# Optimization experiments

Measured on AMD Instinct MI355X. Metric: run time of the kernel, lower is better.

The kernel has to match this reference:

```python
import jax, jax.numpy as jnp
import numpy as np
from jax import lax


def ste_round(x):
    # straight-through round (Brevitas fake-quant)
    return x + lax.stop_gradient(jnp.round(x) - x)


def ste_binary(w):
    # straight-through binarization to {-1, +1}
    b = jnp.where(w >= 0, 1.0, -1.0).astype(w.dtype)
    return w + lax.stop_gradient(b - w)


def quant_identity_2b(x, s):
    # signed 2-bit fake quant: levels {-2,-1,0,1} * s
    return jnp.clip(ste_round(x / s), -2.0, 1.0) * s


def quant_relu_2b(x, s):
    # unsigned 2-bit fake quant after ReLU: levels {0,1,2,3} * s
    return jnp.clip(ste_round(jax.nn.relu(x) / s), 0.0, 3.0) * s


def binary_weight(w, s):
    return ste_binary(w) * s


def conv2d(x, w):
    return lax.conv_general_dilated(x, w, (1, 1), 'VALID',
                                    dimension_numbers=('NCHW', 'OIHW', 'NCHW'))


def maxpool2(x):
    return lax.reduce_window(x, -jnp.inf, lax.max, (1, 1, 2, 2), (1, 1, 2, 2), 'VALID')


def scale_bias(x, scale, bias):
    # BatchNorm2dToQuantScaleBias at inference: per-channel affine
    return x * scale[None, :, None, None] + bias[None, :, None, None]


def setup_inputs() -> dict:
    key = jax.random.key(0)
    ks = jax.random.split(key, 16)
    B = 16384
    d = {
        'x': jax.random.normal(ks[0], (B, 3, 32, 32), jnp.float32),
        'w1': jax.random.normal(ks[1], (6, 3, 5, 5), jnp.float32) * 0.1,
        'b1': jax.random.normal(ks[2], (6,), jnp.float32) * 0.01,
        'w2': jax.random.normal(ks[3], (16, 6, 5, 5), jnp.float32) * 0.1,
        'b2': jax.random.normal(ks[4], (16,), jnp.float32) * 0.01,
        'fw1': jax.random.normal(ks[5], (100, 400), jnp.float32) * 0.05,
        'fb1': jax.random.normal(ks[6], (100,), jnp.float32) * 0.01,
        'fw2': jax.random.normal(ks[7], (50, 100), jnp.float32) * 0.05,
        'fb2': jax.random.normal(ks[8], (50,), jnp.float32) * 0.01,
        'fw3': jax.random.normal(ks[9], (10, 50), jnp.float32) * 0.05,
        'fb3': jax.random.normal(ks[10], (10,), jnp.float32) * 0.01,
        'bn1_scale': jax.random.uniform(ks[11], (6,), jnp.float32, 0.5, 1.5),
        'bn1_bias': jax.random.normal(ks[12], (6,), jnp.float32) * 0.1,
        'bn2_scale': jax.random.uniform(ks[13], (16,), jnp.float32, 0.5, 1.5),
        'bn2_bias': jax.random.normal(ks[14], (16,), jnp.float32) * 0.1,
        's_in': jnp.float32(1.0),
        's_w1': jnp.float32(0.1),
        's_w2': jnp.float32(0.1),
        's_fw1': jnp.float32(0.05),
        's_fw2': jnp.float32(0.05),
        's_fw3': jnp.float32(0.05),
        's_a1': jnp.float32(0.5),
        's_a2': jnp.float32(0.5),
        's_a3': jnp.float32(0.5),
        's_a4': jnp.float32(0.5),
    }
    return d


def reference(x, w1, b1, w2, b2, fw1, fb1, fw2, fb2, fw3, fb3,
              bn1_scale, bn1_bias, bn2_scale, bn2_bias,
              s_in, s_w1, s_w2, s_fw1, s_fw2, s_fw3,
              s_a1, s_a2, s_a3, s_a4):
    # quant_inp (signed 2-bit)
    x = quant_identity_2b(x, s_in)
    # qconv1 (binary weights) -> pool -> BN scale-bias -> 2-bit ReLU
    x = conv2d(x, binary_weight(w1, s_w1)) + b1[None, :, None, None]   # [B,6,28,28]
    x = scale_bias(maxpool2(x), bn1_scale, bn1_bias)                   # [B,6,14,14]
    x = quant_relu_2b(x, s_a1)
    # qconv2 -> BN -> pool -> 2-bit ReLU (pool and BN commute as in code: BN2(pool2(...)))
    x = conv2d(x, binary_weight(w2, s_w2)) + b2[None, :, None, None]   # [B,16,10,10]
    x = scale_bias(maxpool2(x), bn2_scale, bn2_bias)                   # [B,16,5,5]
    x = quant_relu_2b(x, s_a2)
    # flatten -> binary FCs with 2-bit ReLUs
    x = x.reshape(x.shape[0], -1)                                      # [B,400]
    x = quant_relu_2b(x @ binary_weight(fw1, s_fw1).T + fb1, s_a3)     # [B,100]
    x = quant_relu_2b(x @ binary_weight(fw2, s_fw2).T + fb2, s_a4)     # [B,50]
    x = x @ binary_weight(fw3, s_fw3).T + fb3                          # [B,10]
    return x
```

## Files before the change

### kernel.cpp

```cpp
#include <hip/hip_runtime.h>
#include <stdint.h>

typedef uint32_t u32;

#if defined(__has_builtin) && __has_builtin(__builtin_amdgcn_sdot4)
#define SDOT4(a,b,c) __builtin_amdgcn_sdot4((int)(a),(int)(b),(c),false)
#else
__device__ __forceinline__ int sdot4_sw(u32 a, u32 b, int c) {
    c += (int)(int8_t)(a)       * (int)(int8_t)(b);
    c += (int)(int8_t)(a >> 8)  * (int)(int8_t)(b >> 8);
    c += (int)(int8_t)(a >> 16) * (int)(int8_t)(b >> 16);
    c += (int)(int8_t)(a >> 24) * (int)(int8_t)(b >> 24);
    return c;
}
#define SDOT4(a,b,c) sdot4_sw((a),(b),(c))
#endif

__device__ __forceinline__ u32 alignb(u32 hi, u32 lo, unsigned s) {
    return (u32)((((uint64_t)hi << 32) | lo) >> (8u * s));
}
__device__ __forceinline__ u32 sgnb(float v) { return (v >= 0.f) ? 0x01u : 0xFFu; }

__global__ __launch_bounds__(256) void k_prep(
    const float* __restrict__ w1, const float* __restrict__ w2,
    const float* __restrict__ fw1, const float* __restrict__ fw2,
    const float* __restrict__ fw3,
    u32* __restrict__ w1p, u32* __restrict__ w2p, u32* __restrict__ fw1p,
    u32* __restrict__ fw2p, u32* __restrict__ fw3p)
{
    const int tid = threadIdx.x;
    for (int i = tid; i < 90; i += 256) {
        const float* r = w1 + i * 5;
        w1p[i*2]   = sgnb(r[0]) | (sgnb(r[1])<<8) | (sgnb(r[2])<<16) | (sgnb(r[3])<<24);
        w1p[i*2+1] = sgnb(r[4]);
    }
    for (int i = tid; i < 480; i += 256) {
        const float* r = w2 + i * 5;
        w2p[i*2]   = sgnb(r[0]) | (sgnb(r[1])<<8) | (sgnb(r[2])<<16) | (sgnb(r[3])<<24);
        w2p[i*2+1] = sgnb(r[4]);
    }
    for (int i = tid; i < 10000; i += 256) {
        const float* r = fw1 + i * 4;
        fw1p[i] = sgnb(r[0]) | (sgnb(r[1])<<8) | (sgnb(r[2])<<16) | (sgnb(r[3])<<24);
    }
    for (int i = tid; i < 1250; i += 256) {
        const float* r = fw2 + i * 4;
        fw2p[i] = sgnb(r[0]) | (sgnb(r[1])<<8) | (sgnb(r[2])<<16) | (sgnb(r[3])<<24);
    }
    for (int i = tid; i < 130; i += 256) {
        const int o = i / 13, j = i % 13;
        u32 v = 0;
        #pragma unroll
        for (int m = 0; m < 4; ++m) {
            const int k = 4*j + m;
            if (k < 50) v |= sgnb(fw3[o*50 + k]) << (8*m);
        }
        fw3p[i] = v;
    }
}

#define NS1 3
__global__ __launch_bounds__(256) void k_conv1(
    const float* __restrict__ x, const u32* __restrict__ w1p,
    const float* __restrict__ b1, const float* __restrict__ bn1s,
    const float* __restrict__ bn1b, const float* __restrict__ p_sin,
    const float* __restrict__ p_sw1, const float* __restrict__ p_sa1,
    uint8_t* __restrict__ a1, int B)
{
    __shared__ u32 q[NS1*768];
    __shared__ u32 wp[180];
    __shared__ float cb[6], cs[6], cbb[6];
    const int tid = threadIdx.x;
    const long long b0 = (long long)blockIdx.x * NS1;

    const float s_in = p_sin[0], s_a1 = p_sa1[0];
    const float c1 = __fmul_rn(s_in, p_sw1[0]);

    if (tid < 180) wp[tid] = w1p[tid];
    else if (tid >= 192 && tid < 198) {
        const int c = tid - 192;
        cb[c] = b1[c]; cs[c] = bn1s[c]; cbb[c] = bn1b[c];
    }

    const long long wbase = b0 * 768;
    for (int i = tid; i < NS1*768; i += 256) {
        if (wbase + i < (long long)B * 768) {
            const float4 v = *(const float4*)(x + (wbase + i) * 4);
            float r0 = fminf(fmaxf(rintf(__fdiv_rn(v.x, s_in)), -2.f), 1.f);
            float r1 = fminf(fmaxf(rintf(__fdiv_rn(v.y, s_in)), -2.f), 1.f);
            float r2 = fminf(fmaxf(rintf(__fdiv_rn(v.z, s_in)), -2.f), 1.f);
            float r3 = fminf(fmaxf(rintf(__fdiv_rn(v.w, s_in)), -2.f), 1.f);
            q[i] = ((u32)(uint8_t)(int8_t)(int)r0)
                 | ((u32)(uint8_t)(int8_t)(int)r1 << 8)
                 | ((u32)(uint8_t)(int8_t)(int)r2 << 16)
                 | ((u32)(uint8_t)(int8_t)(int)r3 << 24);
        }
    }
    __syncthreads();

    if (tid < NS1*84) {
        const int sl = tid / 84, o = tid % 84, c = o / 14, py = o % 14;
        const long long b = b0 + sl;
        if (b < B) {
            int acc0[28], acc1[28];
            #pragma unroll
            for (int p = 0; p < 28; ++p) { acc0[p] = 0; acc1[p] = 0; }
            #pragma unroll
            for (int ci = 0; ci < 3; ++ci) {
                const u32* base = &q[(sl*3 + ci) * 256];
                const u32* wrow = &wp[(c*3 + ci) * 10];
                #pragma unroll
                for (int ir = 0; ir < 6; ++ir) {
                    const u32* rp = base + (2*py + ir) * 8;
                    const uint4 Wa = *(const uint4*)rp;
                    const uint4 Wb = *(const uint4*)(rp + 4);
                    u32 W8[9] = {Wa.x, Wa.y, Wa.z, Wa.w, Wb.x, Wb.y, Wb.z, Wb.w, 0};
                    u32 e[32];
                    #pragma unroll
                    for (int j = 0; j < 8; ++j) {
                        e[4*j]   = W8[j];
                        e[4*j+1] = alignb(W8[j+1], W8[j], 1);
                        e[4*j+2] = alignb(W8[j+1], W8[j], 2);
                        e[4*j+3] = alignb(W8[j+1], W8[j], 3);
                    }
                    if (ir <= 4) {
                        const u32 wa = wrow[ir*2], wb = wrow[ir*2+1];
                        #pragma unroll
                        for (int p = 0; p < 28; ++p)
                            acc0[p] = SDOT4(wa, e[p], SDOT4(wb, e[p+4], acc0[p]));
                    }
                    if (ir >= 1) {
                        const u32 wa = wrow[(ir-1)*2], wb = wrow[(ir-1)*2+1];
                        #pragma unroll
                        for (int p = 0; p < 28; ++p)
                            acc1[p] = SDOT4(wa, e[p], SDOT4(wb, e[p+4], acc1[p]));
                    }
                }
            }
            u32 ow[4] = {0, 0, 0, 0};
            #pragma unroll
            for (int k = 0; k < 14; ++k) {
                const int m = max(max(acc0[2*k], acc0[2*k+1]),
                                  max(acc1[2*k], acc1[2*k+1]));
                const float y = __fadd_rn(__fmul_rn((float)m, c1), cb[c]);
                const float z = __fadd_rn(__fmul_rn(y, cs[c]), cbb[c]);
                const float t = __fdiv_rn(fmaxf(z, 0.f), s_a1);
                const int code = (int)fminf(fmaxf(rintf(t), 0.f), 3.f);
                ow[k >> 2] |= (u32)code << (8 * (k & 3));
            }
            *(uint4*)(a1 + ((size_t)(b*6 + c)*14 + py) * 16) =
                make_uint4(ow[0], ow[1], ow[2], ow[3]);
        }
    }
}

#define NS2 3
__global__ __launch_bounds__(256) void k_conv2(
    const uint8_t* __restrict__ a1, const u32* __restrict__ w2p,
    const float* __restrict__ b2, const float* __restrict__ bn2s,
    const float* __restrict__ bn2b, const float* __restrict__ p_sa1,
    const float* __restrict__ p_sw2, const float* __restrict__ p_sa2,
    uint8_t* __restrict__ a2, int B)
{
    __shared__ u32 aL[NS2*336];
    __shared__ u32 wp[960];
    __shared__ float cb[16], cs[16], cbb[16];
    const int tid = threadIdx.x;
    const long long b0 = (long long)blockIdx.x * NS2;

    const float c2 = __fmul_rn(p_sa1[0], p_sw2[0]);
    const float s_a2 = p_sa2[0];

    for (int i = tid; i < 960; i += 256) wp[i] = w2p[i];
    if (tid < 16) { cb[tid] = b2[tid]; cs[tid] = bn2s[tid]; cbb[tid] = bn2b[tid]; }

    const u32* a1w = (const u32*)a1;
    const long long wbase = b0 * 336;
    for (int i = tid; i < NS2*336; i += 256)
        if (wbase + i < (long long)B * 336) aL[i] = a1w[wbase + i];
    __syncthreads();

    if (tid < NS2*80) {
        const int sl = tid / 80, o = tid % 80, c = o / 5, py = o % 5;
        const long long b = b0 + sl;
        if (b < B) {
            int acc0[10], acc1[10];
            #pragma unroll
            for (int p = 0; p < 10; ++p) { acc0[p] = 0; acc1[p] = 0; }
            #pragma unroll
            for (int ci = 0; ci < 6; ++ci) {
                const u32* base = &aL[sl*336 + ci*56];
                const u32* wrow = &wp[(c*6 + ci) * 10];
                #pragma unroll
                for (int ir = 0; ir < 6; ++ir) {
                    const uint4 Wv = *(const uint4*)(base + (2*py + ir) * 4);
                    u32 W5[5] = {Wv.x, Wv.y, Wv.z, Wv.w, 0};
                    u32 e[14];
                    #pragma unroll
                    for (int j = 0; j < 4; ++j) {
                        e[4*j] = W5[j];
                        if (4*j+1 < 14) e[4*j+1] = alignb(W5[j+1], W5[j], 1);
                        if (4*j+2 < 14) e[4*j+2] = alignb(W5[j+1], W5[j], 2);
                        if (4*j+3 < 14) e[4*j+3] = alignb(W5[j+1], W5[j], 3);
                    }
                    if (ir <= 4) {
                        const u32 wa = wrow[ir*2], wb = wrow[ir*2+1];
                        #pragma unroll
                        for (int p = 0; p < 10; ++p)
                            acc0[p] = SDOT4(wa, e[p], SDOT4(wb, e[p+4], acc0[p]));
                    }
                    if (ir >= 1) {
                        const u32 wa = wrow[(ir-1)*2], wb = wrow[(ir-1)*2+1];
                        #pragma unroll
                        for (int p = 0; p < 10; ++p)
                            acc1[p] = SDOT4(wa, e[p], SDOT4(wb, e[p+4], acc1[p]));
                    }
                }
            }
            uint8_t* op = a2 + (size_t)b * 400 + c * 25 + py * 5;
            #pragma unroll
            for (int k = 0; k < 5; ++k) {
                const int m = max(max(acc0[2*k], acc0[2*k+1]),
                                  max(acc1[2*k], acc1[2*k+1]));
                const float y = __fadd_rn(__fmul_rn((float)m, c2), cb[c]);
                const float z = __fadd_rn(__fmul_rn(y, cs[c]), cbb[c]);
                const float t = __fdiv_rn(fmaxf(z, 0.f), s_a2);
                op[k] = (uint8_t)(int)fminf(fmaxf(rintf(t), 0.f), 3.f);
            }
        }
    }
}

__global__ __launch_bounds__(256) void k_fc(
    const uint8_t* __restrict__ a2,
    const u32* __restrict__ fw1p, const float* __restrict__ fb1,
    const u32* __restrict__ fw2p, const float* __restrict__ fb2,
    const u32* __restrict__ fw3p, const float* __restrict__ fb3,
    const float* __restrict__ p_sa2, const float* __restrict__ p_sfw1,
    const float* __restrict__ p_sfw2, const float* __restrict__ p_sfw3,
    const float* __restrict__ p_sa3, const float* __restrict__ p_sa4,
    float* __restrict__ out, int B)
{
    __shared__ u32 w1L[10000];
    __shared__ u32 w2L[1250];
    __shared__ u32 w3L[130];
    __shared__ float bb1[100], bb2[52], bb3[12];
    __shared__ u32 xw[16*100];
    __shared__ u32 h1w[16*25];
    __shared__ u32 h2w[16*13];
    const int tid = threadIdx.x;
    const long long b0 = (long long)blockIdx.x * 16;

    for (int i = tid; i < 10000; i += 256) w1L[i] = fw1p[i];
    for (int i = tid; i < 1250; i += 256) w2L[i] = fw2p[i];
    if (tid < 130) w3L[tid] = fw3p[tid];
    if (tid < 100) bb1[tid] = fb1[tid];
    else if (tid >= 128 && tid < 178) bb2[tid-128] = fb2[tid-128];
    else if (tid >= 192 && tid < 202) bb3[tid-192] = fb3[tid-192];
    else if (tid >= 224 && tid < 240) h2w[(tid-224)*13 + 12] = 0;
    const u32* a2w = (const u32*)a2;
    const long long wbase = b0 * 100;
    for (int i = tid; i < 1600; i += 256)
        if (wbase + i < (long long)B * 100) xw[i] = a2w[wbase + i];

    const float c3 = __fmul_rn(p_sa2[0], p_sfw1[0]);
    const float c4 = __fmul_rn(p_sa3[0], p_sfw2[0]);
    const float c5 = __fmul_rn(p_sa4[0], p_sfw3[0]);
    const float s_a3 = p_sa3[0], s_a4 = p_sa4[0];
    __syncthreads();

    for (int t = tid; t < 1600; t += 256) {
        const int s = t & 15, o = t >> 4;
        int T = 0;
        const u32* wr = &w1L[o*100];
        const u32* xr = &xw[s*100];
        #pragma unroll 10
        for (int j = 0; j < 100; ++j) T = SDOT4(wr[j], xr[j], T);
        const float y  = __fadd_rn(__fmul_rn((float)T, c3), bb1[o]);
        const float t2 = __fdiv_rn(fmaxf(y, 0.f), s_a3);
        ((uint8_t*)h1w)[s*100 + o] = (uint8_t)(int)fminf(fmaxf(rintf(t2), 0.f), 3.f);
    }
    __syncthreads();

    for (int t = tid; t < 800; t += 256) {
        const int s = t & 15, o = t >> 4;
        int T = 0;
        const u32* wr = &w2L[o*25];
        const u32* xr = &h1w[s*25];
        #pragma unroll
        for (int j = 0; j < 25; ++j) T = SDOT4(wr[j], xr[j], T);
        const float y  = __fadd_rn(__fmul_rn((float)T, c4), bb2[o]);
        const float t2 = __fdiv_rn(fmaxf(y, 0.f), s_a4);
        ((uint8_t*)h2w)[s*52 + o] = (uint8_t)(int)fminf(fmaxf(rintf(t2), 0.f), 3.f);
    }
    __syncthreads();

    for (int t = tid; t < 160; t += 256) {
        const int s = t & 15, o = t >> 4;
        if (b0 + s < B) {
            int T = 0;
            const u32* wr = &w3L[o*13];
            const u32* xr = &h2w[s*13];
            #pragma unroll
            for (int j = 0; j < 13; ++j) T = SDOT4(wr[j], xr[j], T);
            out[(size_t)(b0 + s)*10 + o] = __fadd_rn(__fmul_rn((float)T, c5), bb3[o]);
        }
    }
}

extern "C" void kernel_launch(void* const* d_in, const int* in_sizes, int n_in,
                              void* d_out, int out_size, void* d_ws, size_t ws_size,
                              hipStream_t stream)
{
    const float* x    = (const float*)d_in[0];
    const float* w1   = (const float*)d_in[1];
    const float* b1   = (const float*)d_in[2];
    const float* w2   = (const float*)d_in[3];
    const float* b2   = (const float*)d_in[4];
    const float* fw1  = (const float*)d_in[5];
    const float* fb1  = (const float*)d_in[6];
    const float* fw2  = (const float*)d_in[7];
    const float* fb2  = (const float*)d_in[8];
    const float* fw3  = (const float*)d_in[9];
    const float* fb3  = (const float*)d_in[10];
    const float* bn1s = (const float*)d_in[11];
    const float* bn1b = (const float*)d_in[12];
    const float* bn2s = (const float*)d_in[13];
    const float* bn2b = (const float*)d_in[14];
    const float* s_in = (const float*)d_in[15];
    const float* s_w1 = (const float*)d_in[16];
    const float* s_w2 = (const float*)d_in[17];
    const float* s_fw1= (const float*)d_in[18];
    const float* s_fw2= (const float*)d_in[19];
    const float* s_fw3= (const float*)d_in[20];
    const float* s_a1 = (const float*)d_in[21];
    const float* s_a2 = (const float*)d_in[22];
    const float* s_a3 = (const float*)d_in[23];
    const float* s_a4 = (const float*)d_in[24];

    int B = out_size / 10;
    if (B <= 0) B = 16384;

    uint8_t* ws  = (uint8_t*)d_ws;
    uint8_t* a1  = ws;
    uint8_t* a2  = a1 + (size_t)B * 1344;
    uint8_t* p   = a2 + (size_t)B * 400;
    u32* w1p  = (u32*)p;            p += 180 * 4;
    u32* w2p  = (u32*)p;            p += 960 * 4;
    u32* fw1p = (u32*)p;            p += 10000 * 4;
    u32* fw2p = (u32*)p;            p += 1250 * 4 + 8;
    u32* fw3p = (u32*)p;

    k_prep<<<1, 256, 0, stream>>>(w1, w2, fw1, fw2, fw3,
                                  w1p, w2p, fw1p, fw2p, fw3p);
    const int g1 = (B + NS1 - 1) / NS1;
    k_conv1<<<g1, 256, 0, stream>>>(x, w1p, b1, bn1s, bn1b, s_in, s_w1, s_a1, a1, B);
    const int g2 = (B + NS2 - 1) / NS2;
    k_conv2<<<g2, 256, 0, stream>>>(a1, w2p, b2, bn2s, bn2b, s_a1, s_w2, s_a2, a2, B);
    k_fc<<<(B + 15) / 16, 256, 0, stream>>>(a2, fw1p, fb1, fw2p, fb2, fw3p, fb3,
                                            s_a2, s_fw1, s_fw2, s_fw3, s_a3, s_a4,
                                            (float*)d_out, B);
}
```

Before: 515.6 us.

## Interleave conv1 input channels in LDS and split output rows across two thread halves

Conv1 now stores the quantized input with its three channels interleaved per pixel, so each dot-product word covers channel and x offsets together. Weights are repacked to match, giving 4 full sdot4 words per kernel row instead of 3×2 mostly-padded words. The block grows to 512 threads, each computing half of an output row, which shrinks accumulator arrays and raises parallelism. Results are staged in LDS and written out with coalesced uint4 stores. The price is more LDS, an extra barrier and a more complex shift-selection scheme.

New measurement: 1.042 ms. 102% more time.

```diff
diff --git a/kernel.cpp b/kernel.cpp
--- a/kernel.cpp
+++ b/kernel.cpp
@@ -21,6 +21,11 @@
 }
 __device__ __forceinline__ u32 sgnb(float v) { return (v >= 0.f) ? 0x01u : 0xFFu; }
 
+__device__ __forceinline__ u32 q2b(float v, float s) {
+    const float r = fminf(fmaxf(rintf(__fdiv_rn(v, s)), -2.f), 1.f);
+    return (u32)(uint8_t)(int8_t)(int)r;
+}
+
 __global__ __launch_bounds__(256) void k_prep(
     const float* __restrict__ w1, const float* __restrict__ w2,
     const float* __restrict__ fw1, const float* __restrict__ fw2,
@@ -29,10 +34,18 @@
     u32* __restrict__ fw2p, u32* __restrict__ fw3p)
 {
     const int tid = threadIdx.x;
-    for (int i = tid; i < 90; i += 256) {
-        const float* r = w1 + i * 5;
-        w1p[i*2]   = sgnb(r[0]) | (sgnb(r[1])<<8) | (sgnb(r[2])<<16) | (sgnb(r[3])<<24);
-        w1p[i*2+1] = sgnb(r[4]);
+    for (int i = tid; i < 120; i += 256) {
+        const int c = i / 20, r = i % 20, ky = r / 4, w = r % 4;
+        u32 v = 0;
+        #pragma unroll
+        for (int m = 0; m < 4; ++m) {
+            const int j = 4*w + m;
+            if (j < 15) {
+                const int dx = j / 3, ci = j % 3;
+                v |= sgnb(w1[c*75 + ci*25 + ky*5 + dx]) << (8*m);
+            }
+        }
+        w1p[i] = v;
     }
     for (int i = tid; i < 480; i += 256) {
         const float* r = w2 + i * 5;
@@ -60,15 +73,83 @@
 }
 
 #define NS1 3
-__global__ __launch_bounds__(256) void k_conv1(
+
+template<int G>
+__device__ __forceinline__ void conv1_body(
+    const u32* __restrict__ qs, const u32* __restrict__ wp,
+    const float* __restrict__ cb, const float* __restrict__ cs,
+    const float* __restrict__ cbb,
+    float c1, float s_a1, int c, int py, uint8_t* __restrict__ stb)
+{
+    int acc0[14], acc1[14];
+    #pragma unroll
+    for (int t = 0; t < 14; ++t) { acc0[t] = 0; acc1[t] = 0; }
+
+    const u32* wq = wp + c * 20;
+    #pragma unroll
+    for (int ir = 0; ir < 6; ++ir) {
+        const int r = 2 * py + ir;
+        const u32* rp = qs + r * 28 + G * 8;
+        u32 W[17];
+        {
+            const uint4 A  = *(const uint4*)(rp);
+            const uint4 Bv = *(const uint4*)(rp + 4);
+            const uint4 Cv = *(const uint4*)(rp + 8);
+            const uint4 Dv = *(const uint4*)(rp + 12);
+            W[0]=A.x;   W[1]=A.y;   W[2]=A.z;   W[3]=A.w;
+            W[4]=Bv.x;  W[5]=Bv.y;  W[6]=Bv.z;  W[7]=Bv.w;
+            W[8]=Cv.x;  W[9]=Cv.y;  W[10]=Cv.z; W[11]=Cv.w;
+            W[12]=Dv.x; W[13]=Dv.y; W[14]=Dv.z; W[15]=Dv.w;
+            W[16]=0;
+        }
+        u32 e1[16], e2[16], e3[16];
+        #pragma unroll
+        for (int j = 0; j < 16; ++j) {
+            e1[j] = alignb(W[j+1], W[j], 1);
+            e2[j] = alignb(W[j+1], W[j], 2);
+            e3[j] = alignb(W[j+1], W[j], 3);
+        }
+        uint4 wa, wb;
+        if (ir <= 4) wa = *(const uint4*)(wq + ir * 4);
+        if (ir >= 1) wb = *(const uint4*)(wq + (ir - 1) * 4);
+        #pragma unroll
+        for (int t = 0; t < 14; ++t) {
+            const int bb = 3 * (G * 14 + t);
+            const int st = (bb >> 2) - 8 * G;
+            const int s  = bb & 3;
+            #define C1DOT(ARR) \
+              { if (ir <= 4) acc0[t] = SDOT4(wa.w, ARR[st+3], SDOT4(wa.z, ARR[st+2], \
+                                      SDOT4(wa.y, ARR[st+1], SDOT4(wa.x, ARR[st], acc0[t])))); \
+                if (ir >= 1) acc1[t] = SDOT4(wb.w, ARR[st+3], SDOT4(wb.z, ARR[st+2], \
+                                      SDOT4(wb.y, ARR[st+1], SDOT4(wb.x, ARR[st], acc1[t])))); }
+            if      (s == 0) C1DOT(W)
+            else if (s == 1) C1DOT(e1)
+            else if (s == 2) C1DOT(e2)
+            else             C1DOT(e3)
+            #undef C1DOT
+        }
+    }
+    #pragma unroll
+    for (int k = 0; k < 7; ++k) {
+        const int m = max(max(acc0[2*k], acc0[2*k+1]), max(acc1[2*k], acc1[2*k+1]));
+        const float y  = __fadd_rn(__fmul_rn((float)m, c1), cb[c]);
+        const float z  = __fadd_rn(__fmul_rn(y, cs[c]), cbb[c]);
+        const float t2 = __fdiv_rn(fmaxf(z, 0.f), s_a1);
+        stb[G*7 + k] = (uint8_t)(int)fminf(fmaxf(rintf(t2), 0.f), 3.f);
+    }
+    if (G == 1) { stb[14] = 0; stb[15] = 0; }
+}
+
+__global__ __launch_bounds__(512, 4) void k_conv1(
     const float* __restrict__ x, const u32* __restrict__ w1p,
     const float* __restrict__ b1, const float* __restrict__ bn1s,
     const float* __restrict__ bn1b, const float* __restrict__ p_sin,
     const float* __restrict__ p_sw1, const float* __restrict__ p_sa1,
     uint8_t* __restrict__ a1, int B)
 {
-    __shared__ u32 q[NS1*768];
-    __shared__ u32 wp[180];
+    __shared__ __align__(16) u32 q[NS1 * 896];
+    __shared__ __align__(16) u32 wp[120];
+    __shared__ __align__(16) u32 stg[NS1 * 336];
     __shared__ float cb[6], cs[6], cbb[6];
     const int tid = threadIdx.x;
     const long long b0 = (long long)blockIdx.x * NS1;
@@ -76,82 +157,45 @@
     const float s_in = p_sin[0], s_a1 = p_sa1[0];
     const float c1 = __fmul_rn(s_in, p_sw1[0]);
 
-    if (tid < 180) wp[tid] = w1p[tid];
-    else if (tid >= 192 && tid < 198) {
-        const int c = tid - 192;
+    if (tid < 120) wp[tid] = w1p[tid];
+    else if (tid >= 128 && tid < 134) {
+        const int c = tid - 128;
         cb[c] = b1[c]; cs[c] = bn1s[c]; cbb[c] = bn1b[c];
     }
 
-    const long long wbase = b0 * 768;
-    for (int i = tid; i < NS1*768; i += 256) {
-        if (wbase + i < (long long)B * 768) {
-            const float4 v = *(const float4*)(x + (wbase + i) * 4);
-            float r0 = fminf(fmaxf(rintf(__fdiv_rn(v.x, s_in)), -2.f), 1.f);
-            float r1 = fminf(fmaxf(rintf(__fdiv_rn(v.y, s_in)), -2.f), 1.f);
-            float r2 = fminf(fmaxf(rintf(__fdiv_rn(v.z, s_in)), -2.f), 1.f);
-            float r3 = fminf(fmaxf(rintf(__fdiv_rn(v.w, s_in)), -2.f), 1.f);
-            q[i] = ((u32)(uint8_t)(int8_t)(int)r0)
-                 | ((u32)(uint8_t)(int8_t)(int)r1 << 8)
-                 | ((u32)(uint8_t)(int8_t)(int)r2 << 16)
-                 | ((u32)(uint8_t)(int8_t)(int)r3 << 24);
-        }
-    }
-    __syncthreads();
-
-    if (tid < NS1*84) {
-        const int sl = tid / 84, o = tid % 84, c = o / 14, py = o % 14;
-        const long long b = b0 + sl;
-        if (b < B) {
-            int acc0[28], acc1[28];
-            #pragma unroll
-            for (int p = 0; p < 28; ++p) { acc0[p] = 0; acc1[p] = 0; }
-            #pragma unroll
-            for (int ci = 0; ci < 3; ++ci) {
-                const u32* base = &q[(sl*3 + ci) * 256];
-                const u32* wrow = &wp[(c*3 + ci) * 10];
-                #pragma unroll
-                for (int ir = 0; ir < 6; ++ir) {
-                    const u32* rp = base + (2*py + ir) * 8;
-                    const uint4 Wa = *(const uint4*)rp;
-                    const uint4 Wb = *(const uint4*)(rp + 4);
-                    u32 W8[9] = {Wa.x, Wa.y, Wa.z, Wa.w, Wb.x, Wb.y, Wb.z, Wb.w, 0};
-                    u32 e[32];
-                    #pragma unroll
-                    for (int j = 0; j < 8; ++j) {
-                        e[4*j]   = W8[j];
-                        e[4*j+1] = alignb(W8[j+1], W8[j], 1);
-                        e[4*j+2] = alignb(W8[j+1], W8[j], 2);
-                        e[4*j+3] = alignb(W8[j+1], W8[j], 3);
-                    }
-                    if (ir <= 4) {
-                        const u32 wa = wrow[ir*2], wb = wrow[ir*2+1];
-                        #pragma unroll
-                        for (int p = 0; p < 28; ++p)
-                            acc0[p] = SDOT4(wa, e[p], SDOT4(wb, e[p+4], acc0[p]));
-                    }
-                    if (ir >= 1) {
-                        const u32 wa = wrow[(ir-1)*2], wb = wrow[(ir-1)*2+1];
-                        #pragma unroll
-                        for (int p = 0; p < 28; ++p)
-                            acc1[p] = SDOT4(wa, e[p], SDOT4(wb, e[p+4], acc1[p]));
-                    }
-                }
-            }
-            u32 ow[4] = {0, 0, 0, 0};
-            #pragma unroll
-            for (int k = 0; k < 14; ++k) {
-                const int m = max(max(acc0[2*k], acc0[2*k+1]),
-                                  max(acc1[2*k], acc1[2*k+1]));
-                const float y = __fadd_rn(__fmul_rn((float)m, c1), cb[c]);
-                const float z = __fadd_rn(__fmul_rn(y, cs[c]), cbb[c]);
-                const float t = __fdiv_rn(fmaxf(z, 0.f), s_a1);
-                const int code = (int)fminf(fmaxf(rintf(t), 0.f), 3.f);
-                ow[k >> 2] |= (u32)code << (8 * (k & 3));
-            }
-            *(uint4*)(a1 + ((size_t)(b*6 + c)*14 + py) * 16) =
-                make_uint4(ow[0], ow[1], ow[2], ow[3]);
-        }
-    }
+    for (int i = tid; i < NS1 * 256; i += 512) {
+        const int sl = i >> 8, r2 = i & 255, row = r2 >> 3, xq = r2 & 7;
+        if (b0 + sl < B) {
+            const float* px = x + (b0 + sl) * 3072 + row * 32 + xq * 4;
+            const float4 f0 = *(const float4*)(px);
+            const float4 f1 = *(const float4*)(px + 1024);
+            const float4 f2 = *(const float4*)(px + 2048);
+            const u32 b00 = q2b(f0.x, s_in), b01 = q2b(f1.x, s_in), b02 = q2b(f2.x, s_in);
+            const u32 b10 = q2b(f0.y, s_in), b11 = q2b(f1.y, s_in), b12 = q2b(f2.y, s_in);
+            const u32 b20 = q2b(f0.z, s_in), b21 = q2b(f1.z, s_in), b22 = q2b(f2.z, s_in);
+            const u32 b30 = q2b(f0.w, s_in), b31 = q2b(f1.w, s_in), b32 = q2b(f2.w, s_in);
+            u32* qp = q + sl * 896 + row * 28 + xq * 3;
+            qp[0] = b00 | (b01 << 8) | (b02 << 16) | (b10 << 24);
+            qp[1] = b11 | (b12 << 8) | (b20 << 16) | (b21 << 24);
+            qp[2] = b22 | (b30 << 8) | (b31 << 16) | (b32 << 24);
+        }
+    }
+    __syncthreads();
+
+    const int G = tid >> 8, idx = tid & 255;
+    if (idx < 252) {
+        const int sl = idx / 84, rem = idx % 84, py = rem / 6, c = rem % 6;
+        if (b0 + sl < B) {
+            uint8_t* stb = (uint8_t*)stg + ((sl * 6 + c) * 14 + py) * 16;
+            if (G == 0) conv1_body<0>(q + sl*896, wp, cb, cs, cbb, c1, s_a1, c, py, stb);
+            else        conv1_body<1>(q + sl*896, wp, cb, cs, cbb, c1, s_a1, c, py, stb);
+        }
+    }
+    __syncthreads();
+
+    const long long nv = ((long long)B - b0) * 84;
+    if (tid < NS1 * 84 && tid < nv)
+        *(uint4*)(a1 + ((size_t)b0 * 84 + tid) * 16) = ((const uint4*)stg)[tid];
 }
 
 #define NS2 3
@@ -354,7 +398,7 @@
     k_prep<<<1, 256, 0, stream>>>(w1, w2, fw1, fw2, fw3,
                                   w1p, w2p, fw1p, fw2p, fw3p);
     const int g1 = (B + NS1 - 1) / NS1;
-    k_conv1<<<g1, 256, 0, stream>>>(x, w1p, b1, bn1s, bn1b, s_in, s_w1, s_a1, a1, B);
+    k_conv1<<<g1, 512, 0, stream>>>(x, w1p, b1, bn1s, bn1b, s_in, s_w1, s_a1, a1, B);
     const int g2 = (B + NS2 - 1) / NS2;
     k_conv2<<<g2, 256, 0, stream>>>(a1, w2p, b2, bn2s, bn2b, s_a1, s_w2, s_a2, a2, B);
     k_fc<<<(B + 15) / 16, 256, 0, stream>>>(a2, fw1p, fb1, fw2p, fb2, fw3p, fb3,
```

## Compute conv1 with bf16 MFMA instead of int8 sdot4 sliding windows

Applied to the files above, without the earlier changes.

Conv1 now quantizes inputs to bf16 values in a channel-interleaved shared-memory layout and runs the 5x5x3 convolution as 16x16x32 bf16 MFMA ops against binary weights prepacked into bf16 fragments. Results are staged in shared memory and written out with coalesced 16-byte stores. The aim is to move the compute-heavy sdot4 inner loop onto the matrix cores, at the cost of more shared memory, redundant padding lanes and a second barrier. Conv2 also gets a launch-bounds occupancy hint.

After: 486.7 us. -5.6%, faster.

```diff
diff --git a/kernel.cpp b/kernel.cpp
--- a/kernel.cpp
+++ b/kernel.cpp
@@ -2,6 +2,8 @@
 #include <stdint.h>
 
 typedef uint32_t u32;
+typedef __attribute__((ext_vector_type(8))) short bf16x8;
+typedef __attribute__((ext_vector_type(4))) float f32x4;
 
 #if defined(__has_builtin) && __has_builtin(__builtin_amdgcn_sdot4)
 #define SDOT4(a,b,c) __builtin_amdgcn_sdot4((int)(a),(int)(b),(c),false)
@@ -21,18 +23,34 @@
 }
 __device__ __forceinline__ u32 sgnb(float v) { return (v >= 0.f) ? 0x01u : 0xFFu; }
 
+__device__ __forceinline__ u32 qbf(float v, float s) {
+    const float r = fminf(fmaxf(rintf(__fdiv_rn(v, s)), -2.f), 1.f);
+    return __float_as_uint(r) >> 16;
+}
+
 __global__ __launch_bounds__(256) void k_prep(
     const float* __restrict__ w1, const float* __restrict__ w2,
     const float* __restrict__ fw1, const float* __restrict__ fw2,
     const float* __restrict__ fw3,
-    u32* __restrict__ w1p, u32* __restrict__ w2p, u32* __restrict__ fw1p,
+    u32* __restrict__ w1pb, u32* __restrict__ w2p, u32* __restrict__ fw1p,
     u32* __restrict__ fw2p, u32* __restrict__ fw3p)
 {
     const int tid = threadIdx.x;
-    for (int i = tid; i < 90; i += 256) {
-        const float* r = w1 + i * 5;
-        w1p[i*2]   = sgnb(r[0]) | (sgnb(r[1])<<8) | (sgnb(r[2])<<16) | (sgnb(r[3])<<24);
-        w1p[i*2+1] = sgnb(r[4]);
+    for (int i = tid; i < 1280; i += 256) {
+        const int w = i & 3, l = (i >> 2) & 63, ky = i >> 8;
+        const int kg = l >> 4, cc = l & 15;
+        u32 v = 0;
+        #pragma unroll
+        for (int h = 0; h < 2; ++h) {
+            const int k = kg * 8 + w * 2 + h;
+            const int ch = k & 3, dx = k >> 2;
+            if (cc < 6 && dx < 5 && ch < 3) {
+                const u32 s = (w1[cc*75 + ch*25 + ky*5 + dx] >= 0.f) ? 0x3F80u
+                                                                     : 0xBF80u;
+                v |= s << (16 * h);
+            }
+        }
+        w1pb[i] = v;
     }
     for (int i = tid; i < 480; i += 256) {
         const float* r = w2 + i * 5;
@@ -61,14 +79,14 @@
 
 #define NS1 3
 __global__ __launch_bounds__(256) void k_conv1(
-    const float* __restrict__ x, const u32* __restrict__ w1p,
+    const float* __restrict__ x, const u32* __restrict__ w1pb,
     const float* __restrict__ b1, const float* __restrict__ bn1s,
     const float* __restrict__ bn1b, const float* __restrict__ p_sin,
     const float* __restrict__ p_sw1, const float* __restrict__ p_sa1,
     uint8_t* __restrict__ a1, int B)
 {
-    __shared__ u32 q[NS1*768];
-    __shared__ u32 wp[180];
+    __shared__ __align__(16) u32 q[NS1 * 2304];
+    __shared__ __align__(16) u32 stg[NS1 * 336];
     __shared__ float cb[6], cs[6], cbb[6];
     const int tid = threadIdx.x;
     const long long b0 = (long long)blockIdx.x * NS1;
@@ -76,86 +94,93 @@
     const float s_in = p_sin[0], s_a1 = p_sa1[0];
     const float c1 = __fmul_rn(s_in, p_sw1[0]);
 
-    if (tid < 180) wp[tid] = w1p[tid];
-    else if (tid >= 192 && tid < 198) {
-        const int c = tid - 192;
-        cb[c] = b1[c]; cs[c] = bn1s[c]; cbb[c] = bn1b[c];
-    }
-
-    const long long wbase = b0 * 768;
-    for (int i = tid; i < NS1*768; i += 256) {
-        if (wbase + i < (long long)B * 768) {
-            const float4 v = *(const float4*)(x + (wbase + i) * 4);
-            float r0 = fminf(fmaxf(rintf(__fdiv_rn(v.x, s_in)), -2.f), 1.f);
-            float r1 = fminf(fmaxf(rintf(__fdiv_rn(v.y, s_in)), -2.f), 1.f);
-            float r2 = fminf(fmaxf(rintf(__fdiv_rn(v.z, s_in)), -2.f), 1.f);
-            float r3 = fminf(fmaxf(rintf(__fdiv_rn(v.w, s_in)), -2.f), 1.f);
-            q[i] = ((u32)(uint8_t)(int8_t)(int)r0)
-                 | ((u32)(uint8_t)(int8_t)(int)r1 << 8)
-                 | ((u32)(uint8_t)(int8_t)(int)r2 << 16)
-                 | ((u32)(uint8_t)(int8_t)(int)r3 << 24);
-        }
-    }
-    __syncthreads();
-
-    if (tid < NS1*84) {
-        const int sl = tid / 84, o = tid % 84, c = o / 14, py = o % 14;
-        const long long b = b0 + sl;
-        if (b < B) {
-            int acc0[28], acc1[28];
-            #pragma unroll
-            for (int p = 0; p < 28; ++p) { acc0[p] = 0; acc1[p] = 0; }
-            #pragma unroll
-            for (int ci = 0; ci < 3; ++ci) {
-                const u32* base = &q[(sl*3 + ci) * 256];
-                const u32* wrow = &wp[(c*3 + ci) * 10];
-                #pragma unroll
-                for (int ir = 0; ir < 6; ++ir) {
-                    const u32* rp = base + (2*py + ir) * 8;
-                    const uint4 Wa = *(const uint4*)rp;
-                    const uint4 Wb = *(const uint4*)(rp + 4);
-                    u32 W8[9] = {Wa.x, Wa.y, Wa.z, Wa.w, Wb.x, Wb.y, Wb.z, Wb.w, 0};
-                    u32 e[32];
-                    #pragma unroll
-                    for (int j = 0; j < 8; ++j) {
-                        e[4*j]   = W8[j];
-                        e[4*j+1] = alignb(W8[j+1], W8[j], 1);
-                        e[4*j+2] = alignb(W8[j+1], W8[j], 2);
-                        e[4*j+3] = alignb(W8[j+1], W8[j], 3);
-                    }
-                    if (ir <= 4) {
-                        const u32 wa = wrow[ir*2], wb = wrow[ir*2+1];
-                        #pragma unroll
-                        for (int p = 0; p < 28; ++p)
-                            acc0[p] = SDOT4(wa, e[p], SDOT4(wb, e[p+4], acc0[p]));
-                    }
-                    if (ir >= 1) {
-                        const u32 wa = wrow[(ir-1)*2], wb = wrow[(ir-1)*2+1];
-                        #pragma unroll
-                        for (int p = 0; p < 28; ++p)
-                            acc1[p] = SDOT4(wa, e[p], SDOT4(wb, e[p+4], acc1[p]));
-                    }
-                }
-            }
-            u32 ow[4] = {0, 0, 0, 0};
-            #pragma unroll
-            for (int k = 0; k < 14; ++k) {
-                const int m = max(max(acc0[2*k], acc0[2*k+1]),
-                                  max(acc1[2*k], acc1[2*k+1]));
-                const float y = __fadd_rn(__fmul_rn((float)m, c1), cb[c]);
-                const float z = __fadd_rn(__fmul_rn(y, cs[c]), cbb[c]);
-                const float t = __fdiv_rn(fmaxf(z, 0.f), s_a1);
-                const int code = (int)fminf(fmaxf(rintf(t), 0.f), 3.f);
-                ow[k >> 2] |= (u32)code << (8 * (k & 3));
-            }
-            *(uint4*)(a1 + ((size_t)(b*6 + c)*14 + py) * 16) =
-                make_uint4(ow[0], ow[1], ow[2], ow[3]);
-        }
-    }
+    if (tid < 6) { cb[tid] = b1[tid]; cs[tid] = bn1s[tid]; cbb[tid] = bn1b[tid]; }
+
+    const int lane = tid & 63;
+    bf16x8 wf[5];
+    #pragma unroll
+    for (int ky = 0; ky < 5; ++ky) {
+        const uint4 u = *(const uint4*)(w1pb + (ky * 64 + lane) * 4);
+        wf[ky] = __builtin_bit_cast(bf16x8, u);
+    }
+
+    for (int i = tid; i < NS1 * 336; i += 256) stg[i] = 0;
+    for (int i = tid; i < NS1 * 256; i += 256) {
+        const int sl = i >> 8, r2 = i & 255, row = r2 >> 3, j = r2 & 7;
+        q[sl * 2304 + row * 72 + 64 + j] = 0;
+    }
+
+    for (int i = tid; i < NS1 * 256; i += 256) {
+        const int sl = i >> 8, r2 = i & 255, row = r2 >> 3, xq = r2 & 7;
+        if (b0 + sl < B) {
+            const float* px = x + (b0 + sl) * 3072 + row * 32 + xq * 4;
+            const float4 f0 = *(const float4*)(px);
+            const float4 f1 = *(const float4*)(px + 1024);
+            const float4 f2 = *(const float4*)(px + 2048);
+            const u32 w0 = qbf(f0.x, s_in) | (qbf(f1.x, s_in) << 16);
+            const u32 w1_ = qbf(f2.x, s_in);
+            const u32 w2_ = qbf(f0.y, s_in) | (qbf(f1.y, s_in) << 16);
+            const u32 w3_ = qbf(f2.y, s_in);
+            const u32 w4_ = qbf(f0.z, s_in) | (qbf(f1.z, s_in) << 16);
+            const u32 w5_ = qbf(f2.z, s_in);
+            const u32 w6_ = qbf(f0.w, s_in) | (qbf(f1.w, s_in) << 16);
+            const u32 w7_ = qbf(f2.w, s_in);
+            u32* qp = q + sl * 2304 + row * 72 + xq * 8;
+            *(uint4*)(qp)     = make_uint4(w0, w1_, w2_, w3_);
+            *(uint4*)(qp + 4) = make_uint4(w4_, w5_, w6_, w7_);
+        }
+    }
+    __syncthreads();
+
+    const int wid = tid >> 6;
+    const int kg = lane >> 4, c = lane & 15;
+    const uint8_t* qbyte = (const uint8_t*)q;
+    for (int t = wid; t < NS1 * 28; t += 4) {
+        const int sl = t / 28, rem = t % 28, pyr = rem >> 1, xh = rem & 1;
+        if (b0 + sl >= B) continue;
+        const int xm = (lane & 15) + 12 * xh;
+        const uint8_t* ab = qbyte + (size_t)(sl * 32 + 2 * pyr) * 288
+                          + xm * 8 + kg * 16;
+        f32x4 acc0 = {0.f, 0.f, 0.f, 0.f}, acc1 = {0.f, 0.f, 0.f, 0.f};
+        #pragma unroll
+        for (int ky = 0; ky < 5; ++ky) {
+            const uint8_t* p0 = ab + ky * 288;
+            uint2 lo = *(const uint2*)(p0);
+            uint2 hi = *(const uint2*)(p0 + 8);
+            acc0 = __builtin_amdgcn_mfma_f32_16x16x32_bf16(
+                __builtin_bit_cast(bf16x8, make_uint4(lo.x, lo.y, hi.x, hi.y)),
+                wf[ky], acc0, 0, 0, 0);
+            const uint8_t* p1 = p0 + 288;
+            lo = *(const uint2*)(p1);
+            hi = *(const uint2*)(p1 + 8);
+            acc1 = __builtin_amdgcn_mfma_f32_16x16x32_bf16(
+                __builtin_bit_cast(bf16x8, make_uint4(lo.x, lo.y, hi.x, hi.y)),
+                wf[ky], acc1, 0, 0, 0);
+        }
+        if (c < 6 && (xh == 0 || kg > 0)) {
+            const float m0 = fmaxf(fmaxf(acc0[0], acc0[1]), fmaxf(acc1[0], acc1[1]));
+            const float m1 = fmaxf(fmaxf(acc0[2], acc0[3]), fmaxf(acc1[2], acc1[3]));
+            const float y0 = __fadd_rn(__fmul_rn(m0, c1), cb[c]);
+            const float z0 = __fadd_rn(__fmul_rn(y0, cs[c]), cbb[c]);
+            const float t0 = __fdiv_rn(fmaxf(z0, 0.f), s_a1);
+            const float y1 = __fadd_rn(__fmul_rn(m1, c1), cb[c]);
+            const float z1 = __fadd_rn(__fmul_rn(y1, cs[c]), cbb[c]);
+            const float t1 = __fdiv_rn(fmaxf(z1, 0.f), s_a1);
+            const int pc = 6 * xh + 2 * kg;
+            uint8_t* sp = (uint8_t*)stg + ((sl * 6 + c) * 14 + pyr) * 16;
+            sp[pc]     = (uint8_t)(int)fminf(fmaxf(rintf(t0), 0.f), 3.f);
+            sp[pc + 1] = (uint8_t)(int)fminf(fmaxf(rintf(t1), 0.f), 3.f);
+        }
+    }
+    __syncthreads();
+
+    const long long nv = ((long long)B - b0) * 84;
+    if (tid < NS1 * 84 && tid < nv)
+        *(uint4*)(a1 + ((size_t)b0 * 84 + tid) * 16) = ((const uint4*)stg)[tid];
 }
 
 #define NS2 3
-__global__ __launch_bounds__(256) void k_conv2(
+__global__ __launch_bounds__(256, 3) void k_conv2(
     const uint8_t* __restrict__ a1, const u32* __restrict__ w2p,
     const float* __restrict__ b2, const float* __restrict__ bn2s,
     const float* __restrict__ bn2b, const float* __restrict__ p_sa1,
@@ -345,16 +370,16 @@
     uint8_t* a1  = ws;
     uint8_t* a2  = a1 + (size_t)B * 1344;
     uint8_t* p   = a2 + (size_t)B * 400;
-    u32* w1p  = (u32*)p;            p += 180 * 4;
+    u32* w1pb = (u32*)p;            p += 1280 * 4;
     u32* w2p  = (u32*)p;            p += 960 * 4;
     u32* fw1p = (u32*)p;            p += 10000 * 4;
     u32* fw2p = (u32*)p;            p += 1250 * 4 + 8;
     u32* fw3p = (u32*)p;
 
     k_prep<<<1, 256, 0, stream>>>(w1, w2, fw1, fw2, fw3,
-                                  w1p, w2p, fw1p, fw2p, fw3p);
+                                  w1pb, w2p, fw1p, fw2p, fw3p);
     const int g1 = (B + NS1 - 1) / NS1;
-    k_conv1<<<g1, 256, 0, stream>>>(x, w1p, b1, bn1s, bn1b, s_in, s_w1, s_a1, a1, B);
+    k_conv1<<<g1, 256, 0, stream>>>(x, w1pb, b1, bn1s, bn1b, s_in, s_w1, s_a1, a1, B);
     const int g2 = (B + NS2 - 1) / NS2;
     k_conv2<<<g2, 256, 0, stream>>>(a1, w2p, b2, bn2s, bn2b, s_a1, s_w2, s_a2, a2, B);
     k_fc<<<(B + 15) / 16, 256, 0, stream>>>(a2, fw1p, fb1, fw2p, fb2, fw3p, fb3,
```
